# Kernel optimization log

Hardware: AMD Instinct MI355X
Metric: run time of the kernel (lower is better)

Reference implementation:

```python
import jax, jax.numpy as jnp
import numpy as np

B = 65536
IN_F = 1024
OUT_F = 1024
N_ACT = 4  # len(activation_functions): tanh, sin, relu, sigmoid (cyclic over columns)


def setup_inputs() -> dict:
    key = jax.random.key(0)
    k1, k2 = jax.random.split(key)
    x = jax.random.normal(k1, (B, IN_F), dtype=jnp.float32)
    # xavier_uniform for weight [out, in]
    limit = float(np.sqrt(6.0 / (IN_F + OUT_F)))
    W = jax.random.uniform(k2, (OUT_F, IN_F), dtype=jnp.float32, minval=-limit, maxval=limit)
    b = jnp.zeros((OUT_F,), dtype=jnp.float32)
    return {"input": x, "W": W, "b": b}


def _apply_cyclic_acts(y):
    # column i gets activation (i % N_ACT); OUT_F % N_ACT == 0 so reshape to groups
    Bb, O = y.shape
    yg = y.reshape(Bb, O // N_ACT, N_ACT)
    out = jnp.stack([
        jnp.tanh(yg[..., 0]),
        jnp.sin(yg[..., 1]),
        jax.nn.relu(yg[..., 2]),
        jax.nn.sigmoid(yg[..., 3]),
    ], axis=-1)
    return out.reshape(Bb, O)


def reference(input, W, b) -> jnp.ndarray:
    y = jnp.einsum('bi,oi->bo', input, W) + b  # F.linear
    return _apply_cyclic_acts(y)
```

## Files before the change

### kernel.cpp

```cpp
#include <hip/hip_runtime.h>

constexpr int B_ROWS = 65536;
constexpr int IN_F   = 1024;
constexpr int OUT_F  = 1024;

constexpr int BDIM = 256;
constexpr int BM = 128, BN = 128, BK = 32;
constexpr int LDK = 40;

typedef __bf16 bf16x8 __attribute__((ext_vector_type(8)));
typedef float  f32x4  __attribute__((ext_vector_type(4)));

__device__ __forceinline__ bf16x8 cvt8(f32x4 u0, f32x4 u1) {
    bf16x8 v;
    v[0] = (__bf16)u0[0]; v[1] = (__bf16)u0[1]; v[2] = (__bf16)u0[2]; v[3] = (__bf16)u0[3];
    v[4] = (__bf16)u1[0]; v[5] = (__bf16)u1[1]; v[6] = (__bf16)u1[2]; v[7] = (__bf16)u1[3];
    return v;
}

__global__ __launch_bounds__(BDIM, 2)
void fused_linear_act(const float* __restrict__ X,
                      const float* __restrict__ W,
                      const float* __restrict__ bias,
                      float* __restrict__ O)
{
    __shared__ __attribute__((aligned(16))) __bf16 As[BM * LDK];
    __shared__ __attribute__((aligned(16))) __bf16 Bs[BN * LDK];

    const int bx = blockIdx.x;
    const int nt = bx & 7;
    const int mt = bx >> 3;
    const int m0 = mt * BM;
    const int n0 = nt * BN;

    const int tid  = threadIdx.x;
    const int lane = tid & 63;
    const int wave = tid >> 6;
    const int wm = (wave >> 1) * 64;
    const int wn = (wave & 1) * 64;
    const int lrow = lane & 15;
    const int quad = lane >> 4;

    const int srow = tid >> 2;
    const int sseg = tid & 3;

    f32x4 acc[4][4];
    #pragma unroll
    for (int i = 0; i < 4; ++i)
        #pragma unroll
        for (int j = 0; j < 4; ++j)
            acc[i][j] = (f32x4){0.f, 0.f, 0.f, 0.f};

    const float* xa = X + (size_t)(m0 + srow)      * IN_F + sseg * 8;
    const float* xb = X + (size_t)(m0 + srow + 64) * IN_F + sseg * 8;
    const float* wa = W + (size_t)(n0 + srow)      * IN_F + sseg * 8;
    const float* wb = W + (size_t)(n0 + srow + 64) * IN_F + sseg * 8;

    __bf16* as0 = &As[(srow)      * LDK + sseg * 8];
    __bf16* as1 = &As[(srow + 64) * LDK + sseg * 8];
    __bf16* bs0 = &Bs[(srow)      * LDK + sseg * 8];
    __bf16* bs1 = &Bs[(srow + 64) * LDK + sseg * 8];

    const __bf16* aBase = &As[(wm + lrow) * LDK + quad * 8];
    const __bf16* bBase = &Bs[(wn + lrow) * LDK + quad * 8];

    for (int k0 = 0; k0 < IN_F; k0 += BK) {
        f32x4 a00 = *(const f32x4*)(xa);     f32x4 a01 = *(const f32x4*)(xa + 4);
        f32x4 a10 = *(const f32x4*)(xb);     f32x4 a11 = *(const f32x4*)(xb + 4);
        f32x4 b00 = *(const f32x4*)(wa);     f32x4 b01 = *(const f32x4*)(wa + 4);
        f32x4 b10 = *(const f32x4*)(wb);     f32x4 b11 = *(const f32x4*)(wb + 4);
        xa += BK; xb += BK; wa += BK; wb += BK;

        __syncthreads();

        *(bf16x8*)as0 = cvt8(a00, a01);
        *(bf16x8*)as1 = cvt8(a10, a11);
        *(bf16x8*)bs0 = cvt8(b00, b01);
        *(bf16x8*)bs1 = cvt8(b10, b11);

        __syncthreads();

        bf16x8 af[4], bf[4];
        #pragma unroll
        for (int t = 0; t < 4; ++t) af[t] = *(const bf16x8*)(aBase + t * 16 * LDK);
        #pragma unroll
        for (int t = 0; t < 4; ++t) bf[t] = *(const bf16x8*)(bBase + t * 16 * LDK);

        #pragma unroll
        for (int i = 0; i < 4; ++i)
            #pragma unroll
            for (int j = 0; j < 4; ++j)
                acc[i][j] = __builtin_amdgcn_mfma_f32_16x16x32_bf16(af[i], bf[j], acc[i][j], 0, 0, 0);
    }

    const int s = lane & 3;
    const float kmul = (s == 0) ? -2.f : -1.f;
    const float aa   = (s == 0) ?  2.f :  1.f;
    const float cc   = (s == 0) ? -1.f :  0.f;
    const bool  is_sin  = (s == 1);
    const bool  is_relu = (s == 2);

    #pragma unroll
    for (int j = 0; j < 4; ++j) {
        const int gc = n0 + wn + j * 16 + lrow;
        const float bv = bias[gc];
        #pragma unroll
        for (int i = 0; i < 4; ++i) {
            const int gr0 = m0 + wm + i * 16 + quad * 4;
            float* op = O + (size_t)gr0 * OUT_F + gc;
            #pragma unroll
            for (int r = 0; r < 4; ++r) {
                const float y = acc[i][j][r] + bv;
                const float e = __expf(kmul * y);
                const float g = fmaf(aa, __builtin_amdgcn_rcpf(1.f + e), cc);
                const float sv = __sinf(y);
                const float rv = fmaxf(y, 0.f);
                const float res = is_sin ? sv : (is_relu ? rv : g);
                op[(size_t)r * OUT_F] = res;
            }
        }
    }
}

extern "C" void kernel_launch(void* const* d_in, const int* in_sizes, int n_in,
                              void* d_out, int out_size, void* d_ws, size_t ws_size,
                              hipStream_t stream) {
    const float* X = (const float*)d_in[0];
    const float* W = (const float*)d_in[1];
    const float* b = (const float*)d_in[2];
    float* O = (float*)d_out;

    const int grid = (B_ROWS / BM) * (OUT_F / BN);
    fused_linear_act<<<grid, BDIM, 0, stream>>>(X, W, b, O);
}
```

Measured before the change: 669.9 us.

## Double-buffer LDS with fragment-ordered layout and XCD-aware tile mapping

Switches shared memory to two buffers so each K-step needs only one barrier. Global loads for the next step are issued right after the current LDS stores, overlapping them with the MFMA work. LDS is laid out in MFMA fragment order so each lane reads one contiguous 16-byte slot without padding, and block IDs are remapped so blocks on the same XCD share M tiles for L2 reuse. The wrapped koff causes one redundant prefetch at the end, and the hand-written waitcnt+barrier relies on the double buffer to avoid write-after-read races.

```diff
diff --git a/kernel.cpp b/kernel.cpp
--- a/kernel.cpp
+++ b/kernel.cpp
@@ -6,7 +6,6 @@
 
 constexpr int BDIM = 256;
 constexpr int BM = 128, BN = 128, BK = 32;
-constexpr int LDK = 40;
 
 typedef __bf16 bf16x8 __attribute__((ext_vector_type(8)));
 typedef float  f32x4  __attribute__((ext_vector_type(4)));
@@ -18,18 +17,21 @@
     return v;
 }
 
+#define LDS_SYNC() asm volatile("s_waitcnt lgkmcnt(0)\n\ts_barrier" ::: "memory")
+
 __global__ __launch_bounds__(BDIM, 2)
 void fused_linear_act(const float* __restrict__ X,
                       const float* __restrict__ W,
                       const float* __restrict__ bias,
                       float* __restrict__ O)
 {
-    __shared__ __attribute__((aligned(16))) __bf16 As[BM * LDK];
-    __shared__ __attribute__((aligned(16))) __bf16 Bs[BN * LDK];
+    __shared__ __attribute__((aligned(16))) unsigned char lds[2 * 16384];
 
-    const int bx = blockIdx.x;
-    const int nt = bx & 7;
-    const int mt = bx >> 3;
+    const int bx  = blockIdx.x;
+    const int xcd = bx & 7;
+    const int idx = bx >> 3;
+    const int nt  = idx & 7;
+    const int mt  = xcd + 8 * (idx >> 3);
     const int m0 = mt * BM;
     const int n0 = nt * BN;
 
@@ -51,46 +53,58 @@
         for (int j = 0; j < 4; ++j)
             acc[i][j] = (f32x4){0.f, 0.f, 0.f, 0.f};
 
-    const float* xa = X + (size_t)(m0 + srow)      * IN_F + sseg * 8;
-    const float* xb = X + (size_t)(m0 + srow + 64) * IN_F + sseg * 8;
-    const float* wa = W + (size_t)(n0 + srow)      * IN_F + sseg * 8;
-    const float* wb = W + (size_t)(n0 + srow + 64) * IN_F + sseg * 8;
+    const float* xa = X + (size_t)(m0 + srow) * IN_F + sseg * 8;
+    const float* xb = xa + (size_t)64 * IN_F;
+    const float* wa = W + (size_t)(n0 + srow) * IN_F + sseg * 8;
+    const float* wb = wa + (size_t)64 * IN_F;
 
-    __bf16* as0 = &As[(srow)      * LDK + sseg * 8];
-    __bf16* as1 = &As[(srow + 64) * LDK + sseg * 8];
-    __bf16* bs0 = &Bs[(srow)      * LDK + sseg * 8];
-    __bf16* bs1 = &Bs[(srow + 64) * LDK + sseg * 8];
+    unsigned char* wr = &lds[((srow >> 4) * 64 + sseg * 16 + (srow & 15)) * 16];
+    const unsigned char* rdA = &lds[(wm >> 4) * 1024 + lane * 16];
+    const unsigned char* rdB = &lds[8192 + (wn >> 4) * 1024 + lane * 16];
 
-    const __bf16* aBase = &As[(wm + lrow) * LDK + quad * 8];
-    const __bf16* bBase = &Bs[(wn + lrow) * LDK + quad * 8];
+    f32x4 A00, A01, A10, A11, B00, B01, B10, B11;
+    A00 = *(const f32x4*)(xa);     A01 = *(const f32x4*)(xa + 4);
+    A10 = *(const f32x4*)(xb);     A11 = *(const f32x4*)(xb + 4);
+    B00 = *(const f32x4*)(wa);     B01 = *(const f32x4*)(wa + 4);
+    B10 = *(const f32x4*)(wb);     B11 = *(const f32x4*)(wb + 4);
+    int koff = 0;
 
-    for (int k0 = 0; k0 < IN_F; k0 += BK) {
-        f32x4 a00 = *(const f32x4*)(xa);     f32x4 a01 = *(const f32x4*)(xa + 4);
-        f32x4 a10 = *(const f32x4*)(xb);     f32x4 a11 = *(const f32x4*)(xb + 4);
-        f32x4 b00 = *(const f32x4*)(wa);     f32x4 b01 = *(const f32x4*)(wa + 4);
-        f32x4 b10 = *(const f32x4*)(wb);     f32x4 b11 = *(const f32x4*)(wb + 4);
-        xa += BK; xb += BK; wa += BK; wb += BK;
+    auto stage = [&](int buf) {
+        unsigned char* w = wr + buf * 16384;
+        *(bf16x8*)(w +     0) = cvt8(A00, A01);
+        *(bf16x8*)(w +  4096) = cvt8(A10, A11);
+        *(bf16x8*)(w +  8192) = cvt8(B00, B01);
+        *(bf16x8*)(w + 12288) = cvt8(B10, B11);
+        koff = (koff + BK) & (IN_F - 1);
+        A00 = *(const f32x4*)(xa + koff); A01 = *(const f32x4*)(xa + koff + 4);
+        A10 = *(const f32x4*)(xb + koff); A11 = *(const f32x4*)(xb + koff + 4);
+        B00 = *(const f32x4*)(wa + koff); B01 = *(const f32x4*)(wa + koff + 4);
+        B10 = *(const f32x4*)(wb + koff); B11 = *(const f32x4*)(wb + koff + 4);
+    };
 
-        __syncthreads();
-
-        *(bf16x8*)as0 = cvt8(a00, a01);
-        *(bf16x8*)as1 = cvt8(a10, a11);
-        *(bf16x8*)bs0 = cvt8(b00, b01);
-        *(bf16x8*)bs1 = cvt8(b10, b11);
-
-        __syncthreads();
-
-        bf16x8 af[4], bf[4];
+    auto compute = [&](int buf) {
+        const unsigned char* ra = rdA + buf * 16384;
+        const unsigned char* rb = rdB + buf * 16384;
+        bf16x8 af[4], bfr[4];
         #pragma unroll
-        for (int t = 0; t < 4; ++t) af[t] = *(const bf16x8*)(aBase + t * 16 * LDK);
+        for (int t = 0; t < 4; ++t) af[t]  = *(const bf16x8*)(ra + t * 1024);
         #pragma unroll
-        for (int t = 0; t < 4; ++t) bf[t] = *(const bf16x8*)(bBase + t * 16 * LDK);
-
+        for (int t = 0; t < 4; ++t) bfr[t] = *(const bf16x8*)(rb + t * 1024);
         #pragma unroll
         for (int i = 0; i < 4; ++i)
             #pragma unroll
             for (int j = 0; j < 4; ++j)
-                acc[i][j] = __builtin_amdgcn_mfma_f32_16x16x32_bf16(af[i], bf[j], acc[i][j], 0, 0, 0);
+                acc[i][j] = __builtin_amdgcn_mfma_f32_16x16x32_bf16(af[i], bfr[j], acc[i][j], 0, 0, 0);
+    };
+
+    #pragma unroll 1
+    for (int it = 0; it < IN_F / BK; it += 2) {
+        stage(0);
+        LDS_SYNC();
+        compute(0);
+        stage(1);
+        LDS_SYNC();
+        compute(1);
     }
 
     const int s = lane & 3;
```

New measurement: 638.6 us. 4.7% less time.
